# Kernel tuning notes

Measured on AMD Instinct MI355X. Metric: run time of the kernel, lower is better.

Reference implementation:

```python
import jax, jax.numpy as jnp
import numpy as np

N, DIN, DOUT = 8192, 128, 128
NEG = -9.0e15  # the module's -9000000000000000.0 mask value
ALPHA = 0.2    # LeakyReLU negative slope


def setup_inputs() -> dict:
    key = jax.random.key(0)
    kx, ka, kw, ks, kr = jax.random.split(key, 5)
    X = jax.random.normal(kx, (N, DIN), dtype=jnp.float32)
    A = (jax.random.uniform(ka, (N, N)) < 0.01).astype(jnp.float32)
    A = A.at[jnp.arange(N), jnp.arange(N)].set(1.0)
    # Linear weight (Kaiming-uniform-ish range is irrelevant to math; use Xavier)
    lim_w = float(np.sqrt(6.0 / (DIN + DOUT)))
    W = jax.random.uniform(kw, (DOUT, DIN), jnp.float32, -lim_w, lim_w)
    b = jnp.zeros((DOUT,), jnp.float32)
    lim_a = float(np.sqrt(6.0 / (DOUT + 1)))
    a_s = jax.random.uniform(ks, (DOUT, 1), jnp.float32, -lim_a, lim_a)
    a_r = jax.random.uniform(kr, (DOUT, 1), jnp.float32, -lim_a, lim_a)
    return {"X": X, "A": A, "W": W, "b": b, "a_s": a_s, "a_r": a_r}


def reference(X, A, W, b, a_s, a_r):
    # H_in = Linear(X)
    H = X @ W.T + b                         # [N, DOUT]
    s = H @ a_s                             # [N, 1] source scores
    r = H @ a_r                             # [N, 1] receiver scores
    # M_s = A * s (broadcast over cols), M_r = A * r^T (broadcast over rows)
    e = jax.nn.leaky_relu(A * s + A * r.T, negative_slope=ALPHA)  # [N, N]
    masked = jnp.where(A > 0, e, NEG)
    att = jax.nn.softmax(masked, axis=1)    # row-stochastic attention
    H_out = att @ H                         # [N, DOUT]  (act = Identity, dropout = eval)
    # NOTE: the torch module applies LayerNorm into a local var but returns
    # the pre-norm H_out, so LayerNorm is dead code. A and [] passthroughs omitted.
    return H_out
```

## Files before the change

kernel.cpp:

```cpp
#include <hip/hip_runtime.h>

#define N 8192
#define D 128
#define ALPHA 0.2f
#define RCAP 256

typedef float fx4 __attribute__((ext_vector_type(4)));

__global__ __launch_bounds__(256) void linear_kernel(
    const float* __restrict__ X, const float* __restrict__ W,
    const float* __restrict__ b, const float* __restrict__ a_s,
    const float* __restrict__ a_r,
    float* __restrict__ H, float* __restrict__ sv, float* __restrict__ rv)
{
    __shared__ float Xs[128 * 36];
    __shared__ float Ws[64 * 132];

    const int tid = threadIdx.x;
    const int i0  = blockIdx.x * 32;

    for (int idx = tid; idx < 32 * 128; idx += 256) {
        const int row = idx >> 7, k = idx & 127;
        Xs[k * 36 + row] = X[(i0 + row) * D + k];
    }

    float acc[4][4] = {};
    const int ty = tid >> 5, tx = tid & 31;
    const int rbase = ty * 4, cbase = tx * 4;

    for (int kb = 0; kb < 2; ++kb) {
        __syncthreads();
        for (int idx = tid; idx < 64 * 128; idx += 256) {
            const int o = idx >> 6, kk = idx & 63;
            Ws[kk * 132 + o] = W[o * D + kb * 64 + kk];
        }
        __syncthreads();
        #pragma unroll
        for (int kk = 0; kk < 64; ++kk) {
            const float4 xv = *(const float4*)&Xs[(kb * 64 + kk) * 36 + rbase];
            const float4 wv = *(const float4*)&Ws[kk * 132 + cbase];
            const float xr[4] = {xv.x, xv.y, xv.z, xv.w};
            const float wc[4] = {wv.x, wv.y, wv.z, wv.w};
            #pragma unroll
            for (int r = 0; r < 4; ++r)
                #pragma unroll
                for (int c = 0; c < 4; ++c)
                    acc[r][c] += xr[r] * wc[c];
        }
    }

    const float4 bv  = *(const float4*)&b[cbase];
    const float4 asv = *(const float4*)&a_s[cbase];
    const float4 arv = *(const float4*)&a_r[cbase];
    #pragma unroll
    for (int r = 0; r < 4; ++r) {
        float4 h;
        h.x = acc[r][0] + bv.x;
        h.y = acc[r][1] + bv.y;
        h.z = acc[r][2] + bv.z;
        h.w = acc[r][3] + bv.w;
        *(float4*)&H[(size_t)(i0 + rbase + r) * D + cbase] = h;
        float ps = h.x * asv.x + h.y * asv.y + h.z * asv.z + h.w * asv.w;
        float pr = h.x * arv.x + h.y * arv.y + h.z * arv.z + h.w * arv.w;
        #pragma unroll
        for (int off = 16; off > 0; off >>= 1) {
            ps += __shfl_xor(ps, off);
            pr += __shfl_xor(pr, off);
        }
        if (tx == 0) {
            sv[i0 + rbase + r] = ps;
            rv[i0 + rbase + r] = pr;
        }
    }
}

__global__ __launch_bounds__(256) void mask_kernel(
    const float* __restrict__ A, unsigned short* __restrict__ Mk)
{
    const int lane = threadIdx.x & 63;
    const int wgid = blockIdx.x * 4 + (threadIdx.x >> 6);
    const fx4* __restrict__ A4 = (const fx4*)A;

    #pragma unroll 2
    for (int it = 0; it < 8; ++it) {
        const int    c  = it * 8192 + wgid;
        const size_t fb = (size_t)c * 256;
        const fx4 a0 = __builtin_nontemporal_load(&A4[fb +   0 + lane]);
        const fx4 a1 = __builtin_nontemporal_load(&A4[fb +  64 + lane]);
        const fx4 a2 = __builtin_nontemporal_load(&A4[fb + 128 + lane]);
        const fx4 a3 = __builtin_nontemporal_load(&A4[fb + 192 + lane]);
        unsigned m = 0;
        m |= (a0.x != 0.0f ? 1u : 0u) << 0;
        m |= (a0.y != 0.0f ? 1u : 0u) << 1;
        m |= (a0.z != 0.0f ? 1u : 0u) << 2;
        m |= (a0.w != 0.0f ? 1u : 0u) << 3;
        m |= (a1.x != 0.0f ? 1u : 0u) << 4;
        m |= (a1.y != 0.0f ? 1u : 0u) << 5;
        m |= (a1.z != 0.0f ? 1u : 0u) << 6;
        m |= (a1.w != 0.0f ? 1u : 0u) << 7;
        m |= (a2.x != 0.0f ? 1u : 0u) << 8;
        m |= (a2.y != 0.0f ? 1u : 0u) << 9;
        m |= (a2.z != 0.0f ? 1u : 0u) << 10;
        m |= (a2.w != 0.0f ? 1u : 0u) << 11;
        m |= (a3.x != 0.0f ? 1u : 0u) << 12;
        m |= (a3.y != 0.0f ? 1u : 0u) << 13;
        m |= (a3.z != 0.0f ? 1u : 0u) << 14;
        m |= (a3.w != 0.0f ? 1u : 0u) << 15;
        Mk[(size_t)c * 64 + lane] = (unsigned short)m;
    }
}

__global__ __launch_bounds__(256, 8) void gather_kernel(
    const unsigned short* __restrict__ Mk, const float* __restrict__ H,
    const float* __restrict__ sv, const float* __restrict__ rv,
    float* __restrict__ out)
{
    __shared__ float2 s_l[4][RCAP];

    const int wave = threadIdx.x >> 6;
    const int lane = threadIdx.x & 63;
    const int i    = blockIdx.x * 4 + wave;

    const uint4 mw = ((const uint4*)(Mk + (size_t)i * 512))[lane];
    unsigned wv[4] = {mw.x, mw.y, mw.z, mw.w};

    const int c = __popc(wv[0]) + __popc(wv[1]) + __popc(wv[2]) + __popc(wv[3]);

    int scan = c;
    #pragma unroll
    for (int off = 1; off < 64; off <<= 1) {
        const int t = __shfl_up(scan, off);
        if (lane >= off) scan += t;
    }
    int base = scan - c;
    int cnt  = __shfl(scan, 63);
    cnt = (cnt < RCAP) ? cnt : RCAP;

    #pragma unroll
    for (int widx = 0; widx < 4; ++widx) {
        unsigned mm = wv[widx];
        while (mm) {
            const int p = __ffs(mm) - 1;
            mm &= mm - 1;
            const int k = lane * 8 + widx * 2 + (p >> 4);
            const int b = p & 15;
            const int col = ((k >> 6) << 10) + ((b >> 2) << 8) + ((k & 63) << 2) + (b & 3);
            if (base < RCAP) s_l[wave][base].y = __int_as_float(col);
            ++base;
        }
    }

    const float si = sv[i];
    float zv[4];
    #pragma unroll
    for (int k = 0; k < 4; ++k) {
        const int p = lane + 64 * k;
        const bool act = (p < cnt);
        const int j = act ? __float_as_int(s_l[wave][p].y) : 0;
        float z = si + rv[j];
        z = (z > 0.0f) ? z : ALPHA * z;
        zv[k] = act ? z : -3.0e38f;
    }
    float lm = fmaxf(fmaxf(zv[0], zv[1]), fmaxf(zv[2], zv[3]));
    #pragma unroll
    for (int off = 32; off > 0; off >>= 1) lm = fmaxf(lm, __shfl_xor(lm, off));

    float sl = 0.0f;
    float wv4[4];
    #pragma unroll
    for (int k = 0; k < 4; ++k) {
        const int p = lane + 64 * k;
        const float w = (p < cnt) ? __expf(zv[k] - lm) : 0.0f;
        wv4[k] = w;
        sl += w;
    }
    #pragma unroll
    for (int off = 32; off > 0; off >>= 1) sl += __shfl_xor(sl, off);
    const float inv = 1.0f / sl;

    #pragma unroll
    for (int k = 0; k < 4; ++k) {
        const int p = lane + 64 * k;
        if (p < cnt) s_l[wave][p].x = wv4[k] * inv;
    }

    const int sub = lane >> 5;
    const int fb  = (lane & 31) * 4;
    float4 acc = make_float4(0.0f, 0.0f, 0.0f, 0.0f);
    #pragma unroll 8
    for (int p = sub; p < cnt; p += 2) {
        const float2 wj = s_l[wave][p];
        const int   j  = __float_as_int(wj.y);
        const float4 h = *(const float4*)&H[(size_t)j * D + fb];
        acc.x += wj.x * h.x;
        acc.y += wj.x * h.y;
        acc.z += wj.x * h.z;
        acc.w += wj.x * h.w;
    }
    acc.x += __shfl_xor(acc.x, 32);
    acc.y += __shfl_xor(acc.y, 32);
    acc.z += __shfl_xor(acc.z, 32);
    acc.w += __shfl_xor(acc.w, 32);
    if (sub == 0)
        *(float4*)&out[(size_t)i * D + fb] = acc;
}

extern "C" void kernel_launch(void* const* d_in, const int* in_sizes, int n_in,
                              void* d_out, int out_size, void* d_ws, size_t ws_size,
                              hipStream_t stream) {
    const float* X   = (const float*)d_in[0];
    const float* A   = (const float*)d_in[1];
    const float* W   = (const float*)d_in[2];
    const float* b   = (const float*)d_in[3];
    const float* a_s = (const float*)d_in[4];
    const float* a_r = (const float*)d_in[5];
    float* out = (float*)d_out;

    float* H  = (float*)d_ws;
    float* sv = H + (size_t)N * D;
    float* rv = sv + N;
    unsigned short* Mk = (unsigned short*)(rv + N);

    linear_kernel<<<256, 256, 0, stream>>>(X, W, b, a_s, a_r, H, sv, rv);
    mask_kernel<<<N / 4, 256, 0, stream>>>(A, Mk);
    gather_kernel<<<N / 4, 256, 0, stream>>>(Mk, H, sv, rv, out);
}
```

Before: 383.5 us.

## Fuse adjacency mask compaction into the attention gather kernel

The separate mask kernel, which packed A into a bitmask in workspace, is removed. Each wave now reads its own adjacency row directly, builds the per-lane bitmask in registers, and goes straight into compaction, softmax and aggregation. This drops one kernel launch and the write and re-read of the bitmask. In exchange, the streaming read of A is now interleaved with gather work per row, and occupancy is set to 6 blocks per SM instead of 8. This may lower overlap of the dominant 256MB A stream.

```diff
diff --git a/kernel.cpp b/kernel.cpp
--- a/kernel.cpp
+++ b/kernel.cpp
@@ -74,21 +74,26 @@
     }
 }
 
-__global__ __launch_bounds__(256) void mask_kernel(
-    const float* __restrict__ A, unsigned short* __restrict__ Mk)
+__global__ __launch_bounds__(256, 6) void attn_fused(
+    const float* __restrict__ A, const float* __restrict__ H,
+    const float* __restrict__ sv, const float* __restrict__ rv,
+    float* __restrict__ out)
 {
+    __shared__ float2 s_l[4][RCAP];
+
+    const int wave = threadIdx.x >> 6;
     const int lane = threadIdx.x & 63;
-    const int wgid = blockIdx.x * 4 + (threadIdx.x >> 6);
-    const fx4* __restrict__ A4 = (const fx4*)A;
-
-    #pragma unroll 2
+    const int i    = blockIdx.x * 4 + wave;
+
+    const fx4* __restrict__ Arow = (const fx4*)(A + (size_t)i * N);
+
+    unsigned wv[4] = {0u, 0u, 0u, 0u};
+    #pragma unroll
     for (int it = 0; it < 8; ++it) {
-        const int    c  = it * 8192 + wgid;
-        const size_t fb = (size_t)c * 256;
-        const fx4 a0 = __builtin_nontemporal_load(&A4[fb +   0 + lane]);
-        const fx4 a1 = __builtin_nontemporal_load(&A4[fb +  64 + lane]);
-        const fx4 a2 = __builtin_nontemporal_load(&A4[fb + 128 + lane]);
-        const fx4 a3 = __builtin_nontemporal_load(&A4[fb + 192 + lane]);
+        const fx4 a0 = __builtin_nontemporal_load(&Arow[it * 256 +   0 + lane]);
+        const fx4 a1 = __builtin_nontemporal_load(&Arow[it * 256 +  64 + lane]);
+        const fx4 a2 = __builtin_nontemporal_load(&Arow[it * 256 + 128 + lane]);
+        const fx4 a3 = __builtin_nontemporal_load(&Arow[it * 256 + 192 + lane]);
         unsigned m = 0;
         m |= (a0.x != 0.0f ? 1u : 0u) << 0;
         m |= (a0.y != 0.0f ? 1u : 0u) << 1;
@@ -106,26 +111,10 @@
         m |= (a3.y != 0.0f ? 1u : 0u) << 13;
         m |= (a3.z != 0.0f ? 1u : 0u) << 14;
         m |= (a3.w != 0.0f ? 1u : 0u) << 15;
-        Mk[(size_t)c * 64 + lane] = (unsigned short)m;
-    }
-}
-
-__global__ __launch_bounds__(256, 8) void gather_kernel(
-    const unsigned short* __restrict__ Mk, const float* __restrict__ H,
-    const float* __restrict__ sv, const float* __restrict__ rv,
-    float* __restrict__ out)
-{
-    __shared__ float2 s_l[4][RCAP];
-
-    const int wave = threadIdx.x >> 6;
-    const int lane = threadIdx.x & 63;
-    const int i    = blockIdx.x * 4 + wave;
-
-    const uint4 mw = ((const uint4*)(Mk + (size_t)i * 512))[lane];
-    unsigned wv[4] = {mw.x, mw.y, mw.z, mw.w};
+        wv[it >> 1] |= m << ((it & 1) * 16);
+    }
 
     const int c = __popc(wv[0]) + __popc(wv[1]) + __popc(wv[2]) + __popc(wv[3]);
-
     int scan = c;
     #pragma unroll
     for (int off = 1; off < 64; off <<= 1) {
@@ -142,9 +131,9 @@
         while (mm) {
             const int p = __ffs(mm) - 1;
             mm &= mm - 1;
-            const int k = lane * 8 + widx * 2 + (p >> 4);
-            const int b = p & 15;
-            const int col = ((k >> 6) << 10) + ((b >> 2) << 8) + ((k & 63) << 2) + (b & 3);
+            const int it = widx * 2 + (p >> 4);
+            const int b  = p & 15;
+            const int col = it * 1024 + ((b >> 2) << 8) + (lane << 2) + (b & 3);
             if (base < RCAP) s_l[wave][base].y = __int_as_float(col);
             ++base;
         }
@@ -219,9 +208,7 @@
     float* H  = (float*)d_ws;
     float* sv = H + (size_t)N * D;
     float* rv = sv + N;
-    unsigned short* Mk = (unsigned short*)(rv + N);
 
     linear_kernel<<<256, 256, 0, stream>>>(X, W, b, a_s, a_r, H, sv, rv);
-    mask_kernel<<<N / 4, 256, 0, stream>>>(A, Mk);
-    gather_kernel<<<N / 4, 256, 0, stream>>>(Mk, H, sv, rv, out);
+    attn_fused<<<N / 4, 256, 0, stream>>>(A, H, sv, rv, out);
 }
```

Result: no change. 379.1 us (-1.2%).
